# Optimization experiments

Measured on AMD Instinct MI355X. Metric: run time of the kernel, lower is better.

The kernel has to match this reference:

```python
import jax, jax.numpy as jnp
import numpy as np

MIN_DISP = -128
MAX_DISP = 0

N, C, H, W = 1, 16, 128, 256


def setup_inputs() -> dict:
    key = jax.random.key(0)
    k1, k2 = jax.random.split(key)
    left = jax.random.normal(k1, (N, C, H, W), dtype=jnp.float32)
    right = jax.random.normal(k2, (N, C, H, W), dtype=jnp.float32)
    return {"left": left, "right": right}


def reference(left, right):
    # Disparities i = MIN_DISP .. MAX_DISP-1 (all negative here).
    # For i < 0 (shift s = -i > 0) the torch code computes
    #   pad_bottom(left[:, :, :H-s, :] - right[:, :, s:, :], s)
    # i.e. out[n, d, c, h, w] = left[n,c,h,w] - right[n,c,h+s,w] if h+s < H else 0.
    n, c, h_dim, w_dim = left.shape
    disps = jnp.arange(MIN_DISP, MAX_DISP)          # [D]
    shifts = -disps                                  # [D], positive shifts
    s_max = int(-MIN_DISP)

    # Pad right along H so shifted reads are in-bounds (zeros past the edge).
    right_pad = jnp.pad(right, ((0, 0), (0, 0), (0, s_max), (0, 0)))
    idx = jnp.arange(h_dim)[None, :] + shifts[:, None]   # [D, H]
    right_shift = right_pad[:, :, idx, :]                # [N, C, D, H, W]

    mask = (idx < h_dim).astype(left.dtype)              # [D, H]
    cost = mask[None, None, :, :, None] * (left[:, :, None, :, :] - right_shift)
    # torch.stack(dim=1) -> [N, D, C, H, W]
    return jnp.transpose(cost, (0, 2, 1, 3, 4))
```

## Files before the change

### kernel.cpp

```cpp
#include <hip/hip_runtime.h>


typedef float f32x4 __attribute__((ext_vector_type(4)));

__device__ __forceinline__ void store_tile(f32x4* __restrict__ out,
                                           const f32x4 (&L)[8],
                                           const f32x4 (&R)[8],
                                           int base) {
#pragma unroll
    for (int ab = -7; ab <= 7; ++ab) {
        const int lo = ab > 0 ? ab : 0;
        const int hi = ab < 0 ? 7 + ab : 7;
#pragma unroll
        for (int a = lo; a <= hi; ++a) {
            const int b = a - ab;
            f32x4 o;
            o.x = L[a].x - R[b].x;
            o.y = L[a].y - R[b].y;
            o.z = L[a].z - R[b].z;
            o.w = L[a].w - R[b].w;
            out[(base + a + ab * 2048) * 64] = o;
        }
    }
}

__global__ __launch_bounds__(256) void CostDifference_kernel(
    const f32x4* __restrict__ left,
    const f32x4* __restrict__ right,
    f32x4* __restrict__ out)
{
    __shared__ f32x4 lds[32][64];
    const int lane = threadIdx.x & 63;
    const int w    = threadIdx.x >> 6;

    const int c = blockIdx.x / 66;
    const int r = blockIdx.x - c * 66;

    if (r < 28) {
        int p = r, I = 0;
        while (p >= 7 - I) { p -= 7 - I; ++I; }
        const int J = I + 1 + p;

        const int base_l = (c * 128 + (I << 4)) * 64 + lane;
        const int base_r = (c * 128 + (J << 4)) * 64 + lane;
#pragma unroll
        for (int k = 0; k < 8; ++k) {
            const int row = (k << 2) + w;
            lds[row][lane] = (row < 16) ? left [base_l + (row << 6)]
                                        : right[base_r + ((row - 16) << 6)];
        }
        __syncthreads();

        const int qa = (w >> 1) & 1, qb = w & 1;
        f32x4 L[8], R[8];
#pragma unroll
        for (int a = 0; a < 8; ++a) L[a] = lds[(qa << 3) + a][lane];
#pragma unroll
        for (int b = 0; b < 8; ++b) R[b] = lds[16 + (qb << 3) + b][lane];

        const int i8 = (I << 4) + (qa << 3);
        const int j8 = (J << 4) + (qb << 3);
        const int base = (128 + i8 - j8) * 2048 + c * 128 + i8;
        store_tile(out + lane, L, R, base);
    } else {
        const int wk = ((r - 28) << 2) | w;
        if (wk < 8) {
            const int i8 = wk << 4, j8 = i8 + 8;
            f32x4 L[8], R[8];
#pragma unroll
            for (int a = 0; a < 8; ++a) L[a] = left [(c * 128 + i8 + a) * 64 + lane];
#pragma unroll
            for (int b = 0; b < 8; ++b) R[b] = right[(c * 128 + j8 + b) * 64 + lane];
            const int base = (128 + i8 - j8) * 2048 + c * 128 + i8;
            store_tile(out + lane, L, R, base);
        } else if (wk < 24) {
            const int i8 = (wk - 8) << 3;
            f32x4 L[8], R[8];
#pragma unroll
            for (int a = 0; a < 8; ++a) L[a] = left [(c * 128 + i8 + a) * 64 + lane];
#pragma unroll
            for (int b = 0; b < 8; ++b) R[b] = right[(c * 128 + i8 + b) * 64 + lane];
            const int base = 128 * 2048 + c * 128 + i8;
#pragma unroll
            for (int ab = -7; ab <= -1; ++ab) {
#pragma unroll
                for (int a = 0; a <= 7 + ab; ++a) {
                    const int b = a - ab;
                    f32x4 o;
                    o.x = L[a].x - R[b].x;
                    o.y = L[a].y - R[b].y;
                    o.z = L[a].z - R[b].z;
                    o.w = L[a].w - R[b].w;
                    out[(base + a + ab * 2048) * 64 + lane] = o;
                }
            }
        } else {
            const int t    = wk - 24;
            const int d    = t >> 1;
            const int half = t & 1;
            const int d2   = 127 - d;
            const int n1   = 128 - d;
            const int start = half ? 65 : 0;
            const int end   = half ? 129 : 65;
            const f32x4 zero = {0.f, 0.f, 0.f, 0.f};

            const int e1 = min(end, n1);
            int rb = (d * 2048 + c * 128 + d + start) * 64 + lane;
            for (int kk = start; kk < e1; ++kk, rb += 64) out[rb] = zero;

            const int s2 = max(start, n1);
            rb = (d2 * 2048 + c * 128 + d2 + (s2 - n1)) * 64 + lane;
            for (int kk = s2; kk < end; ++kk, rb += 64) out[rb] = zero;
        }
    }
}

extern "C" void kernel_launch(void* const* d_in, const int* in_sizes, int n_in,
                              void* d_out, int out_size, void* d_ws, size_t ws_size,
                              hipStream_t stream) {
    const f32x4* left  = (const f32x4*)d_in[0];
    const f32x4* right = (const f32x4*)d_in[1];
    f32x4* out = (f32x4*)d_out;

    CostDifference_kernel<<<1056, 256, 0, stream>>>(left, right, out);
}
```

Measured before the change: 42.21 us.

## Enlarge row tiles to 32 and route diagonal blocks through shared memory

Each block now stages 32 left rows and 32 right rows in LDS instead of 16, and each wave emits four 8x8 output tiles from one loaded L set. Diagonal blocks (I==J) also use LDS, so the separate direct-global-load paths for diagonal tiles go away. Grid shrinks from 1056 to 672 blocks. This cuts redundant global reads but adds load imbalance: diagonal blocks split uneven work across waves (three tiles for waves 0-1, two diagonal half-tiles for waves 2-3). It also doubles LDS use per block.

```diff
diff --git a/kernel.cpp b/kernel.cpp
--- a/kernel.cpp
+++ b/kernel.cpp
@@ -3,7 +3,7 @@
 
 typedef float f32x4 __attribute__((ext_vector_type(4)));
 
-__device__ __forceinline__ void store_tile(f32x4* __restrict__ out,
+__device__ __forceinline__ void store_tile(f32x4* __restrict__ outl,
                                            const f32x4 (&L)[8],
                                            const f32x4 (&R)[8],
                                            int base) {
@@ -19,7 +19,26 @@
             o.y = L[a].y - R[b].y;
             o.z = L[a].z - R[b].z;
             o.w = L[a].w - R[b].w;
-            out[(base + a + ab * 2048) * 64] = o;
+            outl[(base + a + ab * 2048) * 64] = o;
+        }
+    }
+}
+
+__device__ __forceinline__ void store_diag(f32x4* __restrict__ outl,
+                                           const f32x4 (&L)[8],
+                                           const f32x4 (&R)[8],
+                                           int base) {
+#pragma unroll
+    for (int ab = -7; ab <= -1; ++ab) {
+#pragma unroll
+        for (int a = 0; a <= 7 + ab; ++a) {
+            const int b = a - ab;
+            f32x4 o;
+            o.x = L[a].x - R[b].x;
+            o.y = L[a].y - R[b].y;
+            o.z = L[a].z - R[b].z;
+            o.w = L[a].w - R[b].w;
+            outl[(base + a + ab * 2048) * 64] = o;
         }
     }
 }
@@ -29,89 +48,89 @@
     const f32x4* __restrict__ right,
     f32x4* __restrict__ out)
 {
-    __shared__ f32x4 lds[32][64];
+    __shared__ f32x4 lds[64][64];
     const int lane = threadIdx.x & 63;
     const int w    = threadIdx.x >> 6;
 
-    const int c = blockIdx.x / 66;
-    const int r = blockIdx.x - c * 66;
+    const int c = blockIdx.x / 42;
+    const int r = blockIdx.x - c * 42;
 
-    if (r < 28) {
-        int p = r, I = 0;
-        while (p >= 7 - I) { p -= 7 - I; ++I; }
-        const int J = I + 1 + p;
+    if (r < 10) {
+        int I, J;
+        if (r < 6) {
+            int p = r; I = 0;
+            while (p >= 3 - I) { p -= 3 - I; ++I; }
+            J = I + 1 + p;
+        } else {
+            I = J = r - 6;
+        }
 
-        const int base_l = (c * 128 + (I << 4)) * 64 + lane;
-        const int base_r = (c * 128 + (J << 4)) * 64 + lane;
+        const int base_l = (c * 128 + (I << 5)) * 64 + lane;
+        const int base_r = (c * 128 + (J << 5)) * 64 + lane;
 #pragma unroll
-        for (int k = 0; k < 8; ++k) {
+        for (int k = 0; k < 16; ++k) {
             const int row = (k << 2) + w;
-            lds[row][lane] = (row < 16) ? left [base_l + (row << 6)]
-                                        : right[base_r + ((row - 16) << 6)];
+            lds[row][lane] = (row < 32) ? left [base_l + (row << 6)]
+                                        : right[base_r + ((row - 32) << 6)];
         }
         __syncthreads();
 
-        const int qa = (w >> 1) & 1, qb = w & 1;
         f32x4 L[8], R[8];
+        if (r < 6) {
+            const int i8 = (I << 5) + (w << 3);
 #pragma unroll
-        for (int a = 0; a < 8; ++a) L[a] = lds[(qa << 3) + a][lane];
+            for (int a = 0; a < 8; ++a) L[a] = lds[(w << 3) + a][lane];
+            for (int bj = 0; bj < 4; ++bj) {
 #pragma unroll
-        for (int b = 0; b < 8; ++b) R[b] = lds[16 + (qb << 3) + b][lane];
-
-        const int i8 = (I << 4) + (qa << 3);
-        const int j8 = (J << 4) + (qb << 3);
-        const int base = (128 + i8 - j8) * 2048 + c * 128 + i8;
-        store_tile(out + lane, L, R, base);
-    } else {
-        const int wk = ((r - 28) << 2) | w;
-        if (wk < 8) {
-            const int i8 = wk << 4, j8 = i8 + 8;
-            f32x4 L[8], R[8];
+                for (int b = 0; b < 8; ++b) R[b] = lds[32 + (bj << 3) + b][lane];
+                const int j8 = (J << 5) + (bj << 3);
+                store_tile(out + lane, L, R,
+                           (128 + i8 - j8) * 2048 + c * 128 + i8);
+            }
+        } else {
+            if (w < 2) {
+                for (int t = 0; t < 3; ++t) {
+                    const int ai = (w == 0) ? 0 : ((t < 2) ? 1 : 2);
+                    const int bj = (w == 0) ? (t + 1) : ((t < 2) ? (t + 2) : 3);
 #pragma unroll
-            for (int a = 0; a < 8; ++a) L[a] = left [(c * 128 + i8 + a) * 64 + lane];
+                    for (int a = 0; a < 8; ++a) L[a] = lds[(ai << 3) + a][lane];
 #pragma unroll
-            for (int b = 0; b < 8; ++b) R[b] = right[(c * 128 + j8 + b) * 64 + lane];
-            const int base = (128 + i8 - j8) * 2048 + c * 128 + i8;
-            store_tile(out + lane, L, R, base);
-        } else if (wk < 24) {
-            const int i8 = (wk - 8) << 3;
-            f32x4 L[8], R[8];
+                    for (int b = 0; b < 8; ++b) R[b] = lds[32 + (bj << 3) + b][lane];
+                    const int i8 = (I << 5) + (ai << 3);
+                    const int j8 = (I << 5) + (bj << 3);
+                    store_tile(out + lane, L, R,
+                               (128 + i8 - j8) * 2048 + c * 128 + i8);
+                }
+            } else {
+                for (int t = 0; t < 2; ++t) {
+                    const int ai = ((w - 2) << 1) | t;
 #pragma unroll
-            for (int a = 0; a < 8; ++a) L[a] = left [(c * 128 + i8 + a) * 64 + lane];
+                    for (int a = 0; a < 8; ++a) L[a] = lds[(ai << 3) + a][lane];
 #pragma unroll
-            for (int b = 0; b < 8; ++b) R[b] = right[(c * 128 + i8 + b) * 64 + lane];
-            const int base = 128 * 2048 + c * 128 + i8;
-#pragma unroll
-            for (int ab = -7; ab <= -1; ++ab) {
-#pragma unroll
-                for (int a = 0; a <= 7 + ab; ++a) {
-                    const int b = a - ab;
-                    f32x4 o;
-                    o.x = L[a].x - R[b].x;
-                    o.y = L[a].y - R[b].y;
-                    o.z = L[a].z - R[b].z;
-                    o.w = L[a].w - R[b].w;
-                    out[(base + a + ab * 2048) * 64 + lane] = o;
+                    for (int b = 0; b < 8; ++b) R[b] = lds[32 + (ai << 3) + b][lane];
+                    const int i8 = (I << 5) + (ai << 3);
+                    store_diag(out + lane, L, R,
+                               128 * 2048 + c * 128 + i8);
                 }
             }
-        } else {
-            const int t    = wk - 24;
-            const int d    = t >> 1;
-            const int half = t & 1;
-            const int d2   = 127 - d;
-            const int n1   = 128 - d;
-            const int start = half ? 65 : 0;
-            const int end   = half ? 129 : 65;
-            const f32x4 zero = {0.f, 0.f, 0.f, 0.f};
+        }
+    } else {
+        const int t    = ((r - 10) << 2) | w;
+        const int d    = t >> 1;
+        const int half = t & 1;
+        const int d2   = 127 - d;
+        const int n1   = 128 - d;
+        const int start = half ? 65 : 0;
+        const int end   = half ? 129 : 65;
+        const f32x4 zero = {0.f, 0.f, 0.f, 0.f};
 
-            const int e1 = min(end, n1);
-            int rb = (d * 2048 + c * 128 + d + start) * 64 + lane;
-            for (int kk = start; kk < e1; ++kk, rb += 64) out[rb] = zero;
+        const int e1 = min(end, n1);
+        int rb = (d * 2048 + c * 128 + d + start) * 64 + lane;
+        for (int kk = start; kk < e1; ++kk, rb += 64) out[rb] = zero;
 
-            const int s2 = max(start, n1);
-            rb = (d2 * 2048 + c * 128 + d2 + (s2 - n1)) * 64 + lane;
-            for (int kk = s2; kk < end; ++kk, rb += 64) out[rb] = zero;
-        }
+        const int s2 = max(start, n1);
+        rb = (d2 * 2048 + c * 128 + d2 + (s2 - n1)) * 64 + lane;
+        for (int kk = s2; kk < end; ++kk, rb += 64) out[rb] = zero;
     }
 }
 
@@ -122,5 +141,5 @@
     const f32x4* right = (const f32x4*)d_in[1];
     f32x4* out = (f32x4*)d_out;
 
-    CostDifference_kernel<<<1056, 256, 0, stream>>>(left, right, out);
+    CostDifference_kernel<<<672, 256, 0, stream>>>(left, right, out);
 }
```

After: 44.23 us. 4.8% more time.
